# Kernel tuning notes

Measured on AMD Instinct MI355X. Metric: run time of the kernel, lower is better.

The kernel has to match this reference:

```python
import jax, jax.numpy as jnp
import numpy as np

OUT_FEATURES = 8192
IN_FEATURES = 8192
BATCH = 512


def setup_inputs() -> dict:
    key = jax.random.key(0)
    k_x, k_w, k_s = jax.random.split(key, 3)
    x = jax.random.normal(k_x, (BATCH, IN_FEATURES), dtype=jnp.float32)
    # packed int4 weights: each int holds two nibbles (values 0..255)
    packed_weight = jax.random.randint(k_w, (OUT_FEATURES, IN_FEATURES // 2), 0, 256, dtype=jnp.int32)
    # per-output-row scale (positive, as produced by abs-max quantization)
    scale = jax.random.uniform(k_s, (OUT_FEATURES, 1), dtype=jnp.float32) * 0.02 + 1e-4
    return {"x": x, "packed_weight": packed_weight, "scale": scale}


def reference(x, packed_weight, scale):
    # Unpack two 4-bit values per byte: high nibble first (matches torch loop:
    # col i <- packed >> 4 & 15, col i+1 <- packed & 15), then subtract zero-point 8.
    hi = (packed_weight >> 4) & 15
    lo = packed_weight & 15
    q = jnp.stack([hi, lo], axis=-1).reshape(OUT_FEATURES, IN_FEATURES) - 8  # [out, in] int
    w = q.astype(scale.dtype) * scale  # dequantized weight [out, in]
    # linear: y = x @ W^T
    return jnp.einsum('bi,oi->bo', x, w)
```

## Files before the change

### kernel.cpp

```cpp
#include <hip/hip_runtime.h>
#include <cstdint>
#include <cstddef>

#define IN_F 8192
#define OUT_F 8192
#define BATCH 512
#define KSPLIT 4
#define KSLICE (IN_F / KSPLIT)
#define BK 32
#define TILES (KSLICE / BK)
#define BM 256
#define BN 256

typedef __bf16 bf16x8 __attribute__((ext_vector_type(8)));
typedef float floatx4 __attribute__((ext_vector_type(4)));

__device__ __forceinline__ ushort f2bf(float f) {
  uint32_t u = __float_as_uint(f);
  u += 0x7FFFu + ((u >> 16) & 1u);
  return (ushort)(u >> 16);
}

__device__ __forceinline__ uint32_t dq(uint32_t u) {
  return (((u | (u << 20)) >> 4) & 0x000F000Fu) | 0x43004300u;
}

__device__ __forceinline__ void gl16(const void* g, uint32_t* l) {
  __builtin_amdgcn_global_load_lds(
      (const __attribute__((address_space(1))) uint32_t*)g,
      (__attribute__((address_space(3))) uint32_t*)l, 16, 0, 0);
}

__global__ __launch_bounds__(256) void cvt_rowsum(const float* __restrict__ x,
                                                  ushort* __restrict__ xb,
                                                  float* __restrict__ rowsum,
                                                  float* __restrict__ zout) {
  const int b = blockIdx.x;
  const int t = threadIdx.x;
  const float4* xr = (const float4*)(x + (size_t)b * IN_F);
  ushort4* xo = (ushort4*)(xb + (size_t)b * IN_F);
  float s[4] = {0.f, 0.f, 0.f, 0.f};
#pragma unroll
  for (int i = 0; i < 8; ++i) {
    float4 v = xr[i * 256 + t];
    ushort4 o;
    o.x = f2bf(v.x); o.y = f2bf(v.y); o.z = f2bf(v.z); o.w = f2bf(v.w);
    xo[i * 256 + t] = o;
    if (zout) {
      float4 z = {0.f, 0.f, 0.f, 0.f};
      ((float4*)(zout + (size_t)b * OUT_F))[i * 256 + t] = z;
    }
    s[i >> 1] += __uint_as_float((uint32_t)o.x << 16) + __uint_as_float((uint32_t)o.y << 16)
               + __uint_as_float((uint32_t)o.z << 16) + __uint_as_float((uint32_t)o.w << 16);
  }
  __shared__ float red[4][4];
  const int lane = t & 63, wid = t >> 6;
#pragma unroll
  for (int j = 0; j < 4; ++j) {
    float v = s[j];
#pragma unroll
    for (int off = 32; off >= 1; off >>= 1) v += __shfl_down(v, off, 64);
    if (lane == 0) red[wid][j] = v;
  }
  __syncthreads();
  if (t < 4) rowsum[t * BATCH + b] = red[0][t] + red[1][t] + red[2][t] + red[3][t];
}

__global__ __launch_bounds__(512, 2) void qgemm(const ushort* __restrict__ xb,
                                                const int* __restrict__ pw,
                                                const float* __restrict__ scale,
                                                const float* __restrict__ rowsum,
                                                float* __restrict__ out,
                                                float* __restrict__ part) {
  __shared__ uint32_t As[4 * 256 * 16];
  __shared__ uint32_t Bs[4 * 256 * 16];

  const int tid = threadIdx.x;
  const int lane = tid & 63;
  const int w = tid >> 6;
  const int wm = w >> 2, wn = w & 3;
  const int lr = lane & 15, lq = lane >> 4;

  const int n0 = blockIdx.x * BN;
  const int m0 = blockIdx.y * BM;
  const int ks = blockIdx.z;

  const int swz = ((lane & 3) ^ ((lane >> 3) & 3)) * 16;
  const char* aSrc0 = (const char*)xb
      + (size_t)(m0 + w * 32 + (lane >> 2)) * (IN_F * 2)
      + (size_t)ks * (KSLICE * 2) + swz;
  const char* bSrc0 = (const char*)pw
      + (size_t)(n0 + w * 32 + (lane >> 2)) * (IN_F * 2)
      + (size_t)ks * (KSLICE * 2) + swz;
  uint32_t* aD = As + w * 512;
  uint32_t* bD = Bs + w * 512;

  const int key = (lr >> 1) & 3;
  const int aBase = wm * 2048 + lr * 16 + ((lq ^ key) * 4);
  const int bBase = wn * 1024 + lr * 16 + ((lq ^ key) * 4);

  floatx4 acc[8][4] = {};

#define BAR() asm volatile("s_barrier" ::: "memory")
#define LGKM0()                                                              \
  asm volatile("s_waitcnt lgkmcnt(0)" ::: "memory");                         \
  __builtin_amdgcn_sched_barrier(0)
#define VMW(n) asm volatile("s_waitcnt vmcnt(" #n ")" ::: "memory")

  gl16(aSrc0, aD);              gl16(aSrc0 + 262144, aD + 256);
  gl16(bSrc0, bD);              gl16(bSrc0 + 262144, bD + 256);
  gl16(aSrc0 + 64, aD + 4096);  gl16(aSrc0 + 64 + 262144, aD + 4096 + 256);
  gl16(bSrc0 + 64, bD + 4096);  gl16(bSrc0 + 64 + 262144, bD + 4096 + 256);
  VMW(4);
  BAR();

  bf16x8 av[4], bv[4];
  int4 pb[4];

  for (int t = 0; t <= TILES - 3; ++t) {
    const int slot = (t & 3) * 4096, wsl = ((t + 2) & 3) * 4096;
    const char* as = aSrc0 + (size_t)(t + 2) * 64;
    const char* bs = bSrc0 + (size_t)(t + 2) * 64;
#pragma unroll
    for (int f = 0; f < 4; ++f)
      pb[f] = *(const int4*)(Bs + slot + bBase + f * 256);
#pragma unroll
    for (int f = 0; f < 4; ++f)
      av[f] = *(const bf16x8*)(As + slot + aBase + f * 256);
    gl16(as, aD + wsl);
    gl16(as + 262144, aD + wsl + 256);
    BAR();
    LGKM0();
#pragma unroll
    for (int f = 0; f < 4; ++f) {
      int4 u;
      u.x = (int)dq((uint32_t)pb[f].x); u.y = (int)dq((uint32_t)pb[f].y);
      u.z = (int)dq((uint32_t)pb[f].z); u.w = (int)dq((uint32_t)pb[f].w);
      bv[f] = *(const bf16x8*)&u;
    }
    __builtin_amdgcn_s_setprio(1);
#pragma unroll
    for (int fm = 0; fm < 4; ++fm)
#pragma unroll
      for (int fn = 0; fn < 4; ++fn)
        acc[fm][fn] = __builtin_amdgcn_mfma_f32_16x16x32_bf16(av[fm], bv[fn],
                                                              acc[fm][fn], 0, 0, 0);
    __builtin_amdgcn_s_setprio(0);
    BAR();
#pragma unroll
    for (int f = 0; f < 4; ++f)
      av[f] = *(const bf16x8*)(As + slot + aBase + 1024 + f * 256);
    gl16(bs, bD + wsl);
    gl16(bs + 262144, bD + wsl + 256);
    BAR();
    LGKM0();
    __builtin_amdgcn_s_setprio(1);
#pragma unroll
    for (int fm = 0; fm < 4; ++fm)
#pragma unroll
      for (int fn = 0; fn < 4; ++fn)
        acc[4 + fm][fn] = __builtin_amdgcn_mfma_f32_16x16x32_bf16(av[fm], bv[fn],
                                                                  acc[4 + fm][fn], 0, 0, 0);
    __builtin_amdgcn_s_setprio(0);
    VMW(4);
    BAR();
  }

  {
    const int slot = ((TILES - 2) & 3) * 4096;
#pragma unroll
    for (int f = 0; f < 4; ++f)
      pb[f] = *(const int4*)(Bs + slot + bBase + f * 256);
#pragma unroll
    for (int f = 0; f < 4; ++f)
      av[f] = *(const bf16x8*)(As + slot + aBase + f * 256);
    BAR();
    LGKM0();
#pragma unroll
    for (int f = 0; f < 4; ++f) {
      int4 u;
      u.x = (int)dq((uint32_t)pb[f].x); u.y = (int)dq((uint32_t)pb[f].y);
      u.z = (int)dq((uint32_t)pb[f].z); u.w = (int)dq((uint32_t)pb[f].w);
      bv[f] = *(const bf16x8*)&u;
    }
#pragma unroll
    for (int fm = 0; fm < 4; ++fm)
#pragma unroll
      for (int fn = 0; fn < 4; ++fn)
        acc[fm][fn] = __builtin_amdgcn_mfma_f32_16x16x32_bf16(av[fm], bv[fn],
                                                              acc[fm][fn], 0, 0, 0);
    BAR();
#pragma unroll
    for (int f = 0; f < 4; ++f)
      av[f] = *(const bf16x8*)(As + slot + aBase + 1024 + f * 256);
    LGKM0();
#pragma unroll
    for (int fm = 0; fm < 4; ++fm)
#pragma unroll
      for (int fn = 0; fn < 4; ++fn)
        acc[4 + fm][fn] = __builtin_amdgcn_mfma_f32_16x16x32_bf16(av[fm], bv[fn],
                                                                  acc[4 + fm][fn], 0, 0, 0);
    VMW(0);
    BAR();
  }
  {
    const int slot = ((TILES - 1) & 3) * 4096;
#pragma unroll
    for (int f = 0; f < 4; ++f)
      pb[f] = *(const int4*)(Bs + slot + bBase + f * 256);
#pragma unroll
    for (int f = 0; f < 4; ++f)
      av[f] = *(const bf16x8*)(As + slot + aBase + f * 256);
    LGKM0();
#pragma unroll
    for (int f = 0; f < 4; ++f) {
      int4 u;
      u.x = (int)dq((uint32_t)pb[f].x); u.y = (int)dq((uint32_t)pb[f].y);
      u.z = (int)dq((uint32_t)pb[f].z); u.w = (int)dq((uint32_t)pb[f].w);
      bv[f] = *(const bf16x8*)&u;
    }
#pragma unroll
    for (int fm = 0; fm < 4; ++fm)
#pragma unroll
      for (int fn = 0; fn < 4; ++fn)
        acc[fm][fn] = __builtin_amdgcn_mfma_f32_16x16x32_bf16(av[fm], bv[fn],
                                                              acc[fm][fn], 0, 0, 0);
#pragma unroll
    for (int f = 0; f < 4; ++f)
      av[f] = *(const bf16x8*)(As + slot + aBase + 1024 + f * 256);
    LGKM0();
#pragma unroll
    for (int fm = 0; fm < 4; ++fm)
#pragma unroll
      for (int fn = 0; fn < 4; ++fn)
        acc[4 + fm][fn] = __builtin_amdgcn_mfma_f32_16x16x32_bf16(av[fm], bv[fn],
                                                                  acc[4 + fm][fn], 0, 0, 0);
  }

  const int omb = m0 + wm * 128 + lq * 4;
  const int on = n0 + wn * 64 + lr;
  float scv[4];
#pragma unroll
  for (int fn = 0; fn < 4; ++fn) scv[fn] = scale[on + fn * 16];
  float rsv[8][4];
#pragma unroll
  for (int fmg = 0; fmg < 8; ++fmg)
#pragma unroll
    for (int rr = 0; rr < 4; ++rr)
      rsv[fmg][rr] = rowsum[ks * BATCH + omb + fmg * 16 + rr];

  if (part) {
    float* dst = (ks == 0) ? out : (part + (size_t)(ks - 1) * BATCH * OUT_F);
#pragma unroll
    for (int fmg = 0; fmg < 8; ++fmg)
#pragma unroll
      for (int fn = 0; fn < 4; ++fn) {
        const float s = scv[fn];
        float* op = dst + (size_t)(omb + fmg * 16) * OUT_F + (on + fn * 16);
#pragma unroll
        for (int rr = 0; rr < 4; ++rr)
          op[(size_t)rr * OUT_F] = s * (acc[fmg][fn][rr] - 136.f * rsv[fmg][rr]);
      }
  } else {
#pragma unroll
    for (int fmg = 0; fmg < 8; ++fmg)
#pragma unroll
      for (int fn = 0; fn < 4; ++fn) {
        const float s = scv[fn];
        float* op = out + (size_t)(omb + fmg * 16) * OUT_F + (on + fn * 16);
#pragma unroll
        for (int rr = 0; rr < 4; ++rr)
          atomicAdd(op + (size_t)rr * OUT_F, s * (acc[fmg][fn][rr] - 136.f * rsv[fmg][rr]));
      }
  }
#undef BAR
#undef LGKM0
#undef VMW
}

__global__ __launch_bounds__(256) void reduce_add(float* __restrict__ out,
                                                  const float* __restrict__ part) {
  const size_t n = (size_t)BATCH * OUT_F / 4;
  float4* o4 = (float4*)out;
  const float4* p0 = (const float4*)part;
  const float4* p1 = p0 + n;
  const float4* p2 = p1 + n;
  for (size_t i = (size_t)blockIdx.x * 256 + threadIdx.x; i < n;
       i += (size_t)gridDim.x * 256) {
    float4 a = o4[i];
    float4 b = p0[i], c = p1[i], d = p2[i];
    a.x += b.x + c.x + d.x;
    a.y += b.y + c.y + d.y;
    a.z += b.z + c.z + d.z;
    a.w += b.w + c.w + d.w;
    o4[i] = a;
  }
}

extern "C" void kernel_launch(void* const* d_in, const int* in_sizes, int n_in,
                              void* d_out, int out_size, void* d_ws, size_t ws_size,
                              hipStream_t stream) {
  const float* x = (const float*)d_in[0];
  const int* pw = (const int*)d_in[1];
  const float* scale = (const float*)d_in[2];
  float* out = (float*)d_out;

  ushort* xb = (ushort*)d_ws;
  float* rowsum = (float*)((char*)d_ws + (size_t)8 * 1024 * 1024);
  const size_t need = (size_t)8 * 1024 * 1024 + 65536
      + (size_t)3 * BATCH * OUT_F * sizeof(float);
  float* part = (ws_size >= need)
      ? (float*)((char*)d_ws + (size_t)8 * 1024 * 1024 + 65536)
      : nullptr;

  cvt_rowsum<<<BATCH, 256, 0, stream>>>(x, xb, rowsum, part ? nullptr : out);
  dim3 grid(OUT_F / BN, BATCH / BM, KSPLIT);
  qgemm<<<grid, 512, 0, stream>>>(xb, pw, scale, rowsum, out, part);
  if (part) reduce_add<<<2048, 256, 0, stream>>>(out, part);
}
```

Before: 284.9 us.

## Load packed weights directly into registers, bypassing LDS staging

Packed int4 weight fragments now go straight from global memory into registers, double-buffered across even and odd tiles, instead of being staged through a shared-memory buffer. Only activations still go through LDS. This cuts LDS traffic and capacity, removes one LDS array and one barrier per tile, and simplifies the pipeline into a macro-unrolled loop. The cost is higher register pressure from 8 int4 prefetch registers. Each warp group also issues redundant global loads of B, since waves with the same wn read the same rows, so L2 traffic rises.

```diff
diff --git a/kernel.cpp b/kernel.cpp
--- a/kernel.cpp
+++ b/kernel.cpp
@@ -23,6 +23,13 @@
 
 __device__ __forceinline__ uint32_t dq(uint32_t u) {
   return (((u | (u << 20)) >> 4) & 0x000F000Fu) | 0x43004300u;
+}
+
+__device__ __forceinline__ bf16x8 dq8(int4 p) {
+  int4 u;
+  u.x = (int)dq((uint32_t)p.x); u.y = (int)dq((uint32_t)p.y);
+  u.z = (int)dq((uint32_t)p.z); u.w = (int)dq((uint32_t)p.w);
+  return *(bf16x8*)&u;
 }
 
 __device__ __forceinline__ void gl16(const void* g, uint32_t* l) {
@@ -73,7 +80,6 @@
                                                 float* __restrict__ out,
                                                 float* __restrict__ part) {
   __shared__ uint32_t As[4 * 256 * 16];
-  __shared__ uint32_t Bs[4 * 256 * 16];
 
   const int tid = threadIdx.x;
   const int lane = tid & 63;
@@ -89,153 +95,83 @@
   const char* aSrc0 = (const char*)xb
       + (size_t)(m0 + w * 32 + (lane >> 2)) * (IN_F * 2)
       + (size_t)ks * (KSLICE * 2) + swz;
-  const char* bSrc0 = (const char*)pw
-      + (size_t)(n0 + w * 32 + (lane >> 2)) * (IN_F * 2)
-      + (size_t)ks * (KSLICE * 2) + swz;
-  uint32_t* aD = As + w * 512;
-  uint32_t* bD = Bs + w * 512;
+
+  const char* bbase = (const char*)pw + (size_t)(n0 + wn * 64 + lr) * (IN_F * 2)
+      + (size_t)ks * (KSLICE * 2) + lq * 16;
+  const char* bp0 = bbase;
+  const char* bp1 = bbase + (size_t)16 * (IN_F * 2);
+  const char* bp2 = bbase + (size_t)32 * (IN_F * 2);
+  const char* bp3 = bbase + (size_t)48 * (IN_F * 2);
 
   const int key = (lr >> 1) & 3;
   const int aBase = wm * 2048 + lr * 16 + ((lq ^ key) * 4);
-  const int bBase = wn * 1024 + lr * 16 + ((lq ^ key) * 4);
 
   floatx4 acc[8][4] = {};
 
+#define VMW6() asm volatile("s_waitcnt vmcnt(6)" ::: "memory")
+#define VMW0() asm volatile("s_waitcnt vmcnt(0)" ::: "memory")
 #define BAR() asm volatile("s_barrier" ::: "memory")
-#define LGKM0()                                                              \
-  asm volatile("s_waitcnt lgkmcnt(0)" ::: "memory");                         \
-  __builtin_amdgcn_sched_barrier(0)
-#define VMW(n) asm volatile("s_waitcnt vmcnt(" #n ")" ::: "memory")
-
-  gl16(aSrc0, aD);              gl16(aSrc0 + 262144, aD + 256);
-  gl16(bSrc0, bD);              gl16(bSrc0 + 262144, bD + 256);
-  gl16(aSrc0 + 64, aD + 4096);  gl16(aSrc0 + 64 + 262144, aD + 4096 + 256);
-  gl16(bSrc0 + 64, bD + 4096);  gl16(bSrc0 + 64 + 262144, bD + 4096 + 256);
-  VMW(4);
+
+#define TILE(tt, P0, P1, P2, P3, ISS)                                        \
+  {                                                                          \
+    const uint32_t* sA = As + (((tt) & 3) * 4096) + aBase;                   \
+    bf16x8 av[4], bv[4];                                                     \
+    bv[0] = dq8(P0); bv[1] = dq8(P1); bv[2] = dq8(P2); bv[3] = dq8(P3);      \
+    _Pragma("unroll") for (int f = 0; f < 4; ++f)                            \
+        av[f] = *(const bf16x8*)(sA + f * 256);                              \
+    if (ISS) {                                                               \
+      const size_t co = (size_t)((tt) + 2) * 64;                             \
+      P0 = *(const int4*)(bp0 + co); P1 = *(const int4*)(bp1 + co);          \
+      P2 = *(const int4*)(bp2 + co); P3 = *(const int4*)(bp3 + co);          \
+      const char* as_ = aSrc0 + co;                                          \
+      uint32_t* ad_ = As + ((((tt) + 2) & 3) * 4096) + w * 512;              \
+      gl16(as_, ad_);                                                        \
+      gl16(as_ + 262144, ad_ + 256);                                         \
+    }                                                                        \
+    __builtin_amdgcn_s_setprio(1);                                           \
+    _Pragma("unroll") for (int f = 0; f < 4; ++f)                            \
+        _Pragma("unroll") for (int fn = 0; fn < 4; ++fn)                     \
+            acc[f][fn] = __builtin_amdgcn_mfma_f32_16x16x32_bf16(            \
+                av[f], bv[fn], acc[f][fn], 0, 0, 0);                         \
+    __builtin_amdgcn_s_setprio(0);                                           \
+    _Pragma("unroll") for (int f = 0; f < 4; ++f)                            \
+        av[f] = *(const bf16x8*)(sA + 1024 + f * 256);                       \
+    __builtin_amdgcn_s_setprio(1);                                           \
+    _Pragma("unroll") for (int f = 0; f < 4; ++f)                            \
+        _Pragma("unroll") for (int fn = 0; fn < 4; ++fn)                     \
+            acc[4 + f][fn] = __builtin_amdgcn_mfma_f32_16x16x32_bf16(        \
+                av[f], bv[fn], acc[4 + f][fn], 0, 0, 0);                     \
+    __builtin_amdgcn_s_setprio(0);                                           \
+  }
+
+  int4 pE0, pE1, pE2, pE3, pO0, pO1, pO2, pO3;
+
+  {
+    uint32_t* aD = As + w * 512;
+    pE0 = *(const int4*)(bp0); pE1 = *(const int4*)(bp1);
+    pE2 = *(const int4*)(bp2); pE3 = *(const int4*)(bp3);
+    gl16(aSrc0, aD);
+    gl16(aSrc0 + 262144, aD + 256);
+    pO0 = *(const int4*)(bp0 + 64); pO1 = *(const int4*)(bp1 + 64);
+    pO2 = *(const int4*)(bp2 + 64); pO3 = *(const int4*)(bp3 + 64);
+    gl16(aSrc0 + 64, aD + 4096);
+    gl16(aSrc0 + 64 + 262144, aD + 4096 + 256);
+    VMW6();
+    BAR();
+  }
+
+  for (int t = 0; t <= TILES - 4; t += 2) {
+    TILE(t, pE0, pE1, pE2, pE3, true);
+    VMW6();
+    BAR();
+    TILE(t + 1, pO0, pO1, pO2, pO3, true);
+    VMW6();
+    BAR();
+  }
+  TILE(TILES - 2, pE0, pE1, pE2, pE3, false);
+  VMW0();
   BAR();
-
-  bf16x8 av[4], bv[4];
-  int4 pb[4];
-
-  for (int t = 0; t <= TILES - 3; ++t) {
-    const int slot = (t & 3) * 4096, wsl = ((t + 2) & 3) * 4096;
-    const char* as = aSrc0 + (size_t)(t + 2) * 64;
-    const char* bs = bSrc0 + (size_t)(t + 2) * 64;
-#pragma unroll
-    for (int f = 0; f < 4; ++f)
-      pb[f] = *(const int4*)(Bs + slot + bBase + f * 256);
-#pragma unroll
-    for (int f = 0; f < 4; ++f)
-      av[f] = *(const bf16x8*)(As + slot + aBase + f * 256);
-    gl16(as, aD + wsl);
-    gl16(as + 262144, aD + wsl + 256);
-    BAR();
-    LGKM0();
-#pragma unroll
-    for (int f = 0; f < 4; ++f) {
-      int4 u;
-      u.x = (int)dq((uint32_t)pb[f].x); u.y = (int)dq((uint32_t)pb[f].y);
-      u.z = (int)dq((uint32_t)pb[f].z); u.w = (int)dq((uint32_t)pb[f].w);
-      bv[f] = *(const bf16x8*)&u;
-    }
-    __builtin_amdgcn_s_setprio(1);
-#pragma unroll
-    for (int fm = 0; fm < 4; ++fm)
-#pragma unroll
-      for (int fn = 0; fn < 4; ++fn)
-        acc[fm][fn] = __builtin_amdgcn_mfma_f32_16x16x32_bf16(av[fm], bv[fn],
-                                                              acc[fm][fn], 0, 0, 0);
-    __builtin_amdgcn_s_setprio(0);
-    BAR();
-#pragma unroll
-    for (int f = 0; f < 4; ++f)
-      av[f] = *(const bf16x8*)(As + slot + aBase + 1024 + f * 256);
-    gl16(bs, bD + wsl);
-    gl16(bs + 262144, bD + wsl + 256);
-    BAR();
-    LGKM0();
-    __builtin_amdgcn_s_setprio(1);
-#pragma unroll
-    for (int fm = 0; fm < 4; ++fm)
-#pragma unroll
-      for (int fn = 0; fn < 4; ++fn)
-        acc[4 + fm][fn] = __builtin_amdgcn_mfma_f32_16x16x32_bf16(av[fm], bv[fn],
-                                                                  acc[4 + fm][fn], 0, 0, 0);
-    __builtin_amdgcn_s_setprio(0);
-    VMW(4);
-    BAR();
-  }
-
-  {
-    const int slot = ((TILES - 2) & 3) * 4096;
-#pragma unroll
-    for (int f = 0; f < 4; ++f)
-      pb[f] = *(const int4*)(Bs + slot + bBase + f * 256);
-#pragma unroll
-    for (int f = 0; f < 4; ++f)
-      av[f] = *(const bf16x8*)(As + slot + aBase + f * 256);
-    BAR();
-    LGKM0();
-#pragma unroll
-    for (int f = 0; f < 4; ++f) {
-      int4 u;
-      u.x = (int)dq((uint32_t)pb[f].x); u.y = (int)dq((uint32_t)pb[f].y);
-      u.z = (int)dq((uint32_t)pb[f].z); u.w = (int)dq((uint32_t)pb[f].w);
-      bv[f] = *(const bf16x8*)&u;
-    }
-#pragma unroll
-    for (int fm = 0; fm < 4; ++fm)
-#pragma unroll
-      for (int fn = 0; fn < 4; ++fn)
-        acc[fm][fn] = __builtin_amdgcn_mfma_f32_16x16x32_bf16(av[fm], bv[fn],
-                                                              acc[fm][fn], 0, 0, 0);
-    BAR();
-#pragma unroll
-    for (int f = 0; f < 4; ++f)
-      av[f] = *(const bf16x8*)(As + slot + aBase + 1024 + f * 256);
-    LGKM0();
-#pragma unroll
-    for (int fm = 0; fm < 4; ++fm)
-#pragma unroll
-      for (int fn = 0; fn < 4; ++fn)
-        acc[4 + fm][fn] = __builtin_amdgcn_mfma_f32_16x16x32_bf16(av[fm], bv[fn],
-                                                                  acc[4 + fm][fn], 0, 0, 0);
-    VMW(0);
-    BAR();
-  }
-  {
-    const int slot = ((TILES - 1) & 3) * 4096;
-#pragma unroll
-    for (int f = 0; f < 4; ++f)
-      pb[f] = *(const int4*)(Bs + slot + bBase + f * 256);
-#pragma unroll
-    for (int f = 0; f < 4; ++f)
-      av[f] = *(const bf16x8*)(As + slot + aBase + f * 256);
-    LGKM0();
-#pragma unroll
-    for (int f = 0; f < 4; ++f) {
-      int4 u;
-      u.x = (int)dq((uint32_t)pb[f].x); u.y = (int)dq((uint32_t)pb[f].y);
-      u.z = (int)dq((uint32_t)pb[f].z); u.w = (int)dq((uint32_t)pb[f].w);
-      bv[f] = *(const bf16x8*)&u;
-    }
-#pragma unroll
-    for (int fm = 0; fm < 4; ++fm)
-#pragma unroll
-      for (int fn = 0; fn < 4; ++fn)
-        acc[fm][fn] = __builtin_amdgcn_mfma_f32_16x16x32_bf16(av[fm], bv[fn],
-                                                              acc[fm][fn], 0, 0, 0);
-#pragma unroll
-    for (int f = 0; f < 4; ++f)
-      av[f] = *(const bf16x8*)(As + slot + aBase + 1024 + f * 256);
-    LGKM0();
-#pragma unroll
-    for (int fm = 0; fm < 4; ++fm)
-#pragma unroll
-      for (int fn = 0; fn < 4; ++fn)
-        acc[4 + fm][fn] = __builtin_amdgcn_mfma_f32_16x16x32_bf16(av[fm], bv[fn],
-                                                                  acc[4 + fm][fn], 0, 0, 0);
-  }
+  TILE(TILES - 1, pO0, pO1, pO2, pO3, false);
 
   const int omb = m0 + wm * 128 + lq * 4;
   const int on = n0 + wn * 64 + lr;
@@ -273,9 +209,10 @@
           atomicAdd(op + (size_t)rr * OUT_F, s * (acc[fmg][fn][rr] - 136.f * rsv[fmg][rr]));
       }
   }
+#undef TILE
+#undef VMW6
+#undef VMW0
 #undef BAR
-#undef LGKM0
-#undef VMW
 }
 
 __global__ __launch_bounds__(256) void reduce_add(float* __restrict__ out,
```

Measured after the change: 277.9 us. -2.4%, faster.
